# Optimization experiments

Hardware: AMD Instinct MI355X
Metric: run time of the kernel (lower is better)

## Reference

```python
import jax, jax.numpy as jnp
import numpy as np

N = 10000            # nodes
E = 320000           # edges (avg degree 32)
L = 4                # layers
S = 64               # hidden 0e multiplicity
V = 16               # hidden 1o multiplicity
EMB = 32             # node-attr embedding dim
NB = 8               # bessel basis per channel (r and v -> 2*NB edge feats)
MR = 2.5             # max_radius
DEG = 32.0           # num_neighbors
GS = S + V           # gate input scalars: 64 scalars + 16 gates
NW = S * 2 + V * 2 + V * 2   # 192 per-edge tensor-product weights
MAXT = 100           # max atom types


def _semi_unitary(K):
    # Newton-Schulz orthogonalization: K^T K -> I (semi-unitary uplift matrix)
    K = K / jnp.linalg.norm(K)
    for _ in range(10):
        K = 1.5 * K - 0.5 * K @ (K.T @ K)
    return K


def _smooth_cutoff(t):
    u = 2.0 * (t - 1.0)
    y = (1.0 - jnp.cos(jnp.pi * u)) * 0.5
    return jnp.where(u > 0, 0.0, jnp.where(u < -1.0, 1.0, y))


def _edge_geom(d):
    # d: (E,3) edge vector. Returns cutoff-weighted 1x1o SH (component norm) and bessel features.
    r = jnp.linalg.norm(d, axis=1)                       # (E,)
    sh = np.sqrt(3.0) * d / r[:, None]                   # spherical harmonics 1x1o
    attr = _smooth_cutoff(r / MR)[:, None] * sh          # (E,3)
    k = jnp.arange(1, NB + 1, dtype=jnp.float32) * jnp.pi
    feat = np.sqrt(2.0 / MR) * jnp.sin(k * (r / MR)[:, None]) / r[:, None]
    return attr, feat * np.sqrt(NB)                      # (E,3), (E,NB)


def _fctp(s, v, attr, Ws, Wv):
    # FullyConnectedTensorProduct with pure-scalar (0e) node attr == attr-weighted per-irrep linear
    os = jnp.einsum('ni,ne,oie->no', s, attr, Ws) / np.sqrt(s.shape[1] * EMB)
    ov = jnp.einsum('nim,ne,oie->nom', v, attr, Wv) / np.sqrt(v.shape[1] * EMB)
    return os, ov


def _forward(x, node_attr, edge_src, edge_dst, emb_table, PU_K, h, mix,
             si_Ws, si_Wv, sc_Ws, sc_Wv, lin1_Ws, lin1_Wv, lin2_Ws, lin2_Wv,
             fc_W1, fc_b1, fc_W2, fc_b2, fc_W3, fc_b3):
    attr = emb_table[node_attr]                          # (N,EMB)
    K = _semi_unitary(PU_K)                              # (V,2)
    yv = jnp.einsum('ui,nim->num', K, x.reshape(N, 2, 3))  # uplift vectors
    ys = jnp.zeros((N, S), x.dtype)
    ys_old, yv_old = ys, yv
    c_s, c_x = np.sin(np.pi / 8), np.cos(np.pi / 8)
    for i in range(L):
        ar, fr = _edge_geom(x[:, :3][edge_src] - x[:, :3][edge_dst])
        av, fv = _edge_geom(x[:, 3:][edge_src] - x[:, 3:][edge_dst])
        a = jnp.stack([ar, av], axis=1)                  # (E,2,3) = 2x1o edge attr
        ef = jnp.concatenate([fr, fv], axis=1)           # (E,2*NB)
        # radial MLP -> per-edge TP weights
        hd = jax.nn.silu(ef @ fc_W1[i] + fc_b1[i])
        hd = jax.nn.silu(hd @ fc_W2[i] + fc_b2[i])
        w = hd @ fc_W3[i] + fc_b3[i]                     # (E,NW)
        w1 = w[:, :S * 2].reshape(-1, S, 2)
        w2 = w[:, S * 2:S * 2 + V * 2].reshape(-1, V, 2)
        w3 = w[:, S * 2 + V * 2:].reshape(-1, V, 2)
        # conv: lin1 -> gather -> TP -> scatter -> lin2 ; plus self-connection
        fs, fvv = _fctp(ys, yv, attr, lin1_Ws[i], lin1_Wv[i])
        s_src, v_src = fs[edge_src], fvv[edge_src]
        # 0e x 1o -> 1o (uvu)
        o1 = jnp.einsum('euv,eu,evm->eum', w1, s_src, a) / np.sqrt(2.0)   # (E,S,3)
        # 1o x 1o -> 0e (uvu)
        dots = jnp.einsum('eum,evm->euv', v_src, a)
        o2 = jnp.einsum('euv,euv->eu', w2, dots) / np.sqrt(6.0)           # (E,V)
        # 1o x 1o -> 1o (cross, uvu)
        cr = jnp.cross(v_src[:, :, None, :], a[:, None, :, :])            # (E,V,2,3)
        o3 = jnp.einsum('euv,euvm->eum', w3, cr) / 2.0                    # (E,V,3)
        mid_s = jax.ops.segment_sum(o2, edge_dst, num_segments=N) / np.sqrt(DEG)
        mid_v = jax.ops.segment_sum(jnp.concatenate([o1, o3], axis=1), edge_dst,
                                    num_segments=N) / np.sqrt(DEG)        # (N,S+V,3)
        cs2, cv2 = _fctp(mid_s, mid_v, attr, lin2_Ws[i], lin2_Wv[i])      # (N,GS),(N,V,3)
        scs, scv = _fctp(ys, yv, attr, sc_Ws[i], sc_Wv[i])
        conv_s = c_s * scs + c_x * cs2
        conv_v = c_s * scv + c_x * cv2
        # gate: silu scalars, sigmoid gates * gated vectors
        gns = jax.nn.silu(conv_s[:, :S])
        gnv = jax.nn.sigmoid(conv_s[:, S:])[:, :, None] * conv_v
        # self-interaction: per-irrep linear
        sis = ys @ si_Ws[i].T / np.sqrt(S)
        siv = jnp.einsum('oi,nim->nom', si_Wv[i], yv) / np.sqrt(V)
        # leapfrog update
        h2 = h[i] ** 2
        ns = 2.0 * ys - ys_old + h2 * (mix[i] * gns + (mix[i] - 1.0) * sis)
        nv = 2.0 * yv - yv_old + h2 * (mix[i] * gnv + (mix[i] - 1.0) * siv)
        ys_old, yv_old = ys, yv
        ys, yv = ns, nv
        x = jnp.einsum('ui,num->nim', K, yv).reshape(N, 6)   # project
    return x


def setup_inputs() -> dict:
    key = jax.random.key(0)
    ks = jax.random.split(key, 24)
    def g(i, sh, fan=1.0):
        return jax.random.normal(ks[i], sh, dtype=jnp.float32) / np.sqrt(fan)
    edge_src = jax.random.randint(ks[20], (E,), 0, N, dtype=jnp.int32)
    off = jax.random.randint(ks[21], (E,), 1, N, dtype=jnp.int32)
    edge_dst = (edge_src + off) % N                      # guarantees src != dst
    return {
        'x': g(0, (N, 6)),
        'batch': jnp.zeros((N,), jnp.int32),
        'node_attr': jax.random.randint(ks[22], (N,), 0, MAXT, dtype=jnp.int32),
        'edge_src': edge_src,
        'edge_dst': edge_dst,
        'emb_table': g(1, (MAXT, EMB)),
        'PU_K': g(2, (V, 2)),
        'h': jnp.full((L,), 0.01, jnp.float32),
        'mix': jnp.full((L,), 0.5, jnp.float32),
        'si_Ws': g(3, (L, S, S)), 'si_Wv': g(4, (L, V, V)),
        'sc_Ws': g(5, (L, GS, S, EMB)), 'sc_Wv': g(6, (L, V, V, EMB)),
        'lin1_Ws': g(7, (L, S, S, EMB)), 'lin1_Wv': g(8, (L, V, V, EMB)),
        'lin2_Ws': g(9, (L, GS, V, EMB)), 'lin2_Wv': g(10, (L, V, S + V, EMB)),
        'fc_W1': g(11, (L, 2 * NB, 64), 2 * NB), 'fc_b1': jnp.zeros((L, 64), jnp.float32),
        'fc_W2': g(12, (L, 64, 64), 64), 'fc_b2': jnp.zeros((L, 64), jnp.float32),
        'fc_W3': g(13, (L, 64, NW), 64), 'fc_b3': jnp.zeros((L, NW), jnp.float32),
    }


def reference(x, batch, node_attr, edge_src, edge_dst, emb_table, PU_K, h, mix,
              si_Ws, si_Wv, sc_Ws, sc_Wv, lin1_Ws, lin1_Wv, lin2_Ws, lin2_Wv,
              fc_W1, fc_b1, fc_W2, fc_b2, fc_W3, fc_b3):
    return _forward(x, node_attr, edge_src, edge_dst, emb_table, PU_K, h, mix,
                    si_Ws, si_Wv, sc_Ws, sc_Wv, lin1_Ws, lin1_Wv, lin2_Ws, lin2_Wv,
                    fc_W1, fc_b1, fc_W2, fc_b2, fc_W3, fc_b3)
```

## Files before the change

### kernel.cpp

```cpp
#include <hip/hip_runtime.h>
#include <hip/hip_fp8.h>
#include <math.h>

#define NN 10000
#define NE 320000
#define NEP (NE + 64)
#define PI_F 3.14159265358979323846f

typedef __attribute__((ext_vector_type(8))) short short8x;
typedef __attribute__((ext_vector_type(4))) float float4x;

#if defined(__has_builtin)
#if __has_builtin(__builtin_amdgcn_cvt_pk_fp8_f32) && __has_builtin(__builtin_amdgcn_cvt_f32_fp8)
#define HW_FP8 1
#endif
#endif

__device__ __forceinline__ unsigned short f2b(float f) {
    unsigned b = __float_as_uint(f);
    return (unsigned short)((b + 0x7FFFu + ((b >> 16) & 1u)) >> 16);
}
__device__ __forceinline__ float b2f(unsigned short u) {
    return __uint_as_float(((unsigned)u) << 16);
}
__device__ __forceinline__ float silu(float x) {
    return x / (1.f + __expf(-x));
}
__device__ __forceinline__ unsigned char f2e4(float f) {
#ifdef HW_FP8
    int r = __builtin_amdgcn_cvt_pk_fp8_f32(f, f, 0, false);
    return (unsigned char)(r & 0xff);
#else
    __hip_fp8_e4m3 q(f);
    return (unsigned char)q.__x;
#endif
}
__device__ __forceinline__ unsigned short pk2(float lo, float hi) {
#ifdef HW_FP8
    int r = __builtin_amdgcn_cvt_pk_fp8_f32(lo, hi, 0, false);
    return (unsigned short)(r & 0xffff);
#else
    return (unsigned short)((unsigned)f2e4(lo) | ((unsigned)f2e4(hi) << 8));
#endif
}
__device__ __forceinline__ float e42f(unsigned char v) {
#ifdef HW_FP8
    return __builtin_amdgcn_cvt_f32_fp8((int)v, 0);
#else
    __hip_fp8_e4m3 q;
    q.__x = (__hip_fp8_storage_t)v;
    return (float)q;
#endif
}
__device__ __forceinline__ float e4sel(unsigned word, int sel) {
#ifdef HW_FP8
    switch (sel & 3) {
        case 0:  return __builtin_amdgcn_cvt_f32_fp8((int)word, 0);
        case 1:  return __builtin_amdgcn_cvt_f32_fp8((int)word, 1);
        case 2:  return __builtin_amdgcn_cvt_f32_fp8((int)word, 2);
        default: return __builtin_amdgcn_cvt_f32_fp8((int)word, 3);
    }
#else
    return e42f((unsigned char)((word >> (8*(sel & 3))) & 0xffu));
#endif
}

__global__ void k_newton_kernel(const float* __restrict__ PU, float* __restrict__ Kout)
{
    if (threadIdx.x != 0 || blockIdx.x != 0) return;
    float K[32];
    float nrm = 0.f;
    for (int i = 0; i < 32; ++i) { K[i] = PU[i]; nrm += K[i]*K[i]; }
    float inv = 1.0f / sqrtf(nrm);
    for (int i = 0; i < 32; ++i) K[i] *= inv;
    for (int it = 0; it < 10; ++it) {
        float m00 = 0.f, m01 = 0.f, m11 = 0.f;
        for (int u = 0; u < 16; ++u) {
            float a = K[2*u], b = K[2*u+1];
            m00 += a*a; m01 += a*b; m11 += b*b;
        }
        for (int u = 0; u < 16; ++u) {
            float a = K[2*u], b = K[2*u+1];
            K[2*u]   = 1.5f*a - 0.5f*(a*m00 + b*m01);
            K[2*u+1] = 1.5f*b - 0.5f*(a*m01 + b*m11);
        }
    }
    for (int i = 0; i < 32; ++i) Kout[i] = K[i];
}

__global__ __launch_bounds__(256) void init_all_kernel(
    const float* __restrict__ x, const float* __restrict__ K,
    float* __restrict__ xp, float* __restrict__ yv0, float* __restrict__ yv1,
    float* __restrict__ ys0, float* __restrict__ ys1, float* __restrict__ fsb)
{
    int tid = blockIdx.x*256 + threadIdx.x;
    if (tid < NN*8) {
        int n = tid >> 3, c = tid & 7;
        xp[tid] = (c < 6) ? x[n*6 + c] : 0.f;
        return;
    }
    int t2 = tid - NN*8;
    if (t2 < NN*48) {
        int n = t2/48, j = t2%48, u = j/3, m = j%3;
        float v = K[2*u]*x[n*6+m] + K[2*u+1]*x[n*6+3+m];
        yv0[t2] = v; yv1[t2] = v;
        return;
    }
    t2 -= NN*48;
    if (t2 < NN*64) { ys0[t2] = 0.f; ys1[t2] = 0.f; fsb[t2] = 0.f; }
}

__global__ void init_fvv_kernel(const float* __restrict__ yv, const int* __restrict__ types,
                                const float* __restrict__ lin1vT0, float* __restrict__ fvv)
{
    int tid = blockIdx.x*blockDim.x + threadIdx.x;
    if (tid >= NN*48) return;
    int n = tid/48, j = tid%48, o = j/3, m = j%3;
    int t = types[n];
    const float* W = lin1vT0 + (size_t)t*256;
    float acc = 0.f;
    #pragma unroll
    for (int i = 0; i < 16; ++i) acc += yv[n*48 + i*3 + m]*W[i*16 + o];
    fvv[tid] = acc;
}

__device__ __forceinline__ void be_body(const float* __restrict__ W, const float* __restrict__ emb,
                                        float* __restrict__ out, int id, int O, int I, float scale)
{
    int o = id % O; int r = id / O;
    int i = r % I; r /= I;
    int t = r % 100; int l = r / 100;
    const float* w  = W + (((size_t)l*O + o)*I + i)*32;
    const float* em = emb + (size_t)t*32;
    float acc = 0.f;
    #pragma unroll
    for (int e = 0; e < 32; ++e) acc += w[e]*em[e];
    out[id] = acc*scale;
}

#define PREP_TOTAL (2048000 + 1638400 + 512000 + 512000 + 102400 + 102400 + 49152 + 16384 + 16384 + 8192 + 1024)
__global__ __launch_bounds__(256) void prep_kernel(
    const float* __restrict__ lin1_Ws, const float* __restrict__ lin1_Wv,
    const float* __restrict__ sc_Ws,   const float* __restrict__ sc_Wv,
    const float* __restrict__ lin2_Ws, const float* __restrict__ lin2_Wv,
    const float* __restrict__ si_Ws,   const float* __restrict__ si_Wv,
    const float* __restrict__ fc_W1,   const float* __restrict__ fc_W2,
    const float* __restrict__ fc_W3,   const float* __restrict__ emb,
    float* __restrict__ lin1sT, float* __restrict__ lin1vT,
    float* __restrict__ scsT,   float* __restrict__ scvT,
    float* __restrict__ lin2sT, float* __restrict__ lin2vT,
    float* __restrict__ siWsT,  float* __restrict__ siWvT,
    unsigned short* __restrict__ w1bp, unsigned short* __restrict__ w2bp,
    unsigned short* __restrict__ w3bf)
{
    const float s2048 = 0.022097086912079608f;
    const float s512  = 0.044194173824159216f;
    const float s2560 = 0.019764235376052372f;
    int tid = blockIdx.x*256 + threadIdx.x;
    if (tid < 2048000) { be_body(sc_Ws,   emb, scsT,   tid, 80, 64, s2048); return; }
    tid -= 2048000;
    if (tid < 1638400) { be_body(lin1_Ws, emb, lin1sT, tid, 64, 64, s2048); return; }
    tid -= 1638400;
    if (tid < 512000)  { be_body(lin2_Ws, emb, lin2sT, tid, 80, 16, s512);  return; }
    tid -= 512000;
    if (tid < 512000)  { be_body(lin2_Wv, emb, lin2vT, tid, 16, 80, s2560); return; }
    tid -= 512000;
    if (tid < 102400)  { be_body(lin1_Wv, emb, lin1vT, tid, 16, 16, s512);  return; }
    tid -= 102400;
    if (tid < 102400)  { be_body(sc_Wv,   emb, scvT,   tid, 16, 16, s512);  return; }
    tid -= 102400;
    if (tid < 49152) {
        int o = tid % 64; int r = tid / 64; int i = r % 192; int l = r / 192;
        w3bf[tid] = f2b(fc_W3[((size_t)l*64 + o)*192 + i]);
        return;
    }
    tid -= 49152;
    if (tid < 16384) {
        int o = tid % 64; int r = tid / 64; int i = r % 64; int l = r / 64;
        siWsT[tid] = si_Ws[((size_t)l*64 + o)*64 + i]*0.125f;
        return;
    }
    tid -= 16384;
    if (tid < 16384) {
        int kk = tid % 64; int r = tid / 64; int n = r % 64; int l = r / 64;
        w2bp[tid] = f2b(fc_W2[((size_t)l*64 + kk)*64 + n]);
        return;
    }
    tid -= 16384;
    if (tid < 8192) {
        int kk = tid % 32; int r = tid / 32; int n = r % 64; int l = r / 64;
        float v = (kk < 16) ? fc_W1[((size_t)l*16 + kk)*64 + n] : 0.f;
        w1bp[tid] = f2b(v);
        return;
    }
    tid -= 8192;
    if (tid < 1024) {
        int o = tid % 16; int r = tid / 16; int i = r % 16; int l = r / 16;
        siWvT[tid] = si_Wv[((size_t)l*16 + o)*16 + i]*0.25f;
    }
}

__global__ void hist_kernel(const int* __restrict__ dst, int* __restrict__ deg)
{
    int e = blockIdx.x*256 + threadIdx.x;
    if (e < NE) atomicAdd(&deg[dst[e]], 1);
}

__global__ __launch_bounds__(256) void scan_kernel(const int* __restrict__ deg,
                                                   int* __restrict__ segoff,
                                                   int* __restrict__ cursor)
{
    __shared__ int part[256];
    int tid = threadIdx.x;
    int base = tid*40;
    int s = 0;
    for (int i = 0; i < 40; ++i) { int idx = base+i; if (idx < NN) s += deg[idx]; }
    part[tid] = s;
    __syncthreads();
    for (int o = 1; o < 256; o <<= 1) {
        int v = (tid >= o) ? part[tid-o] : 0;
        __syncthreads();
        part[tid] += v;
        __syncthreads();
    }
    int excl = part[tid] - s;
    for (int i = 0; i < 40; ++i) {
        int idx = base+i;
        if (idx < NN) { segoff[idx] = excl; cursor[idx] = excl; excl += deg[idx]; }
        else if (idx == NN) { segoff[NN] = excl; }
    }
}

__global__ void scatter_kernel(const int* __restrict__ src, const int* __restrict__ dst,
                               int* __restrict__ cursor,
                               int* __restrict__ srcs, int* __restrict__ dsts)
{
    int e = blockIdx.x*256 + threadIdx.x;
    if (e >= NE) return;
    int d = dst[e];
    int p = atomicAdd(&cursor[d], 1);
    srcs[p] = src[e]; dsts[p] = d;
}

__global__ __launch_bounds__(256, 8) void edge_fused_kernel(
    const float* __restrict__ xp,
    const int* __restrict__ srcs, const int* __restrict__ dsts,
    const unsigned short* __restrict__ w1b,
    const float* __restrict__ b1,
    const unsigned short* __restrict__ w2b,
    const float* __restrict__ b2,
    const unsigned short* __restrict__ w3b,
    const float* __restrict__ b3,
    const float* __restrict__ fs, const float* __restrict__ fvv,
    unsigned short* __restrict__ ebuf)
{
    __shared__ __align__(16) unsigned char smem[64*196];
    __shared__ float abuf[64*6];
    unsigned short* hbuf = (unsigned short*)smem;
    unsigned char*  wbuf = smem;
    int lane = threadIdx.x & 63;
    int wid  = threadIdx.x >> 6;
    int eblk = blockIdx.x * 64;
    int row16 = lane & 15, quad = lane >> 4;
    int erow = 16*wid + row16;

    if (lane < 16) {
        int p = eblk + 16*wid + lane;
        int s = srcs[p], d = dsts[p];
        const float4* xs4 = (const float4*)(xp + (size_t)s*8);
        const float4* xd4 = (const float4*)(xp + (size_t)d*8);
        float4 xsa = xs4[0], xsb = xs4[1];
        float4 xda = xd4[0], xdb = xd4[1];
        float a0[3], a1[3], ef[16];
        {
            float d0 = xsa.x-xda.x, d1 = xsa.y-xda.y, d2 = xsa.z-xda.z;
            float r = sqrtf(d0*d0 + d1*d1 + d2*d2);
            float invr = 1.0f/r;
            float u = 0.8f*r - 2.0f;
            float cut = (u > 0.f) ? 0.f : ((u < -1.f) ? 1.f : 0.5f*(1.f - __cosf(PI_F*u)));
            float sc = 1.7320508075688772f*cut*invr;
            a0[0] = sc*d0; a0[1] = sc*d1; a0[2] = sc*d2;
            float fsc = 2.5298221281347035f*invr;
            #pragma unroll
            for (int k = 0; k < 8; ++k) ef[k] = fsc*__sinf((k+1)*1.2566370614359172f*r);
        }
        {
            float d0 = xsa.w-xda.w, d1 = xsb.x-xdb.x, d2 = xsb.y-xdb.y;
            float r = sqrtf(d0*d0 + d1*d1 + d2*d2);
            float invr = 1.0f/r;
            float u = 0.8f*r - 2.0f;
            float cut = (u > 0.f) ? 0.f : ((u < -1.f) ? 1.f : 0.5f*(1.f - __cosf(PI_F*u)));
            float sc = 1.7320508075688772f*cut*invr;
            a1[0] = sc*d0; a1[1] = sc*d1; a1[2] = sc*d2;
            float fsc = 2.5298221281347035f*invr;
            #pragma unroll
            for (int k = 0; k < 8; ++k) ef[8+k] = fsc*__sinf((k+1)*1.2566370614359172f*r);
        }
        float* ab = abuf + (16*wid + lane)*6;
        ab[0] = a0[0]; ab[1] = a0[1]; ab[2] = a0[2];
        ab[3] = a1[0]; ab[4] = a1[1]; ab[5] = a1[2];
        unsigned epk[8];
        #pragma unroll
        for (int k = 0; k < 8; ++k)
            epk[k] = (unsigned)f2b(ef[2*k]) | ((unsigned)f2b(ef[2*k+1]) << 16);
        uint4* hr = (uint4*)(hbuf + (16*wid + lane)*72);
        uint4 q0; q0.x = epk[0]; q0.y = epk[1]; q0.z = epk[2]; q0.w = epk[3];
        uint4 q1; q1.x = epk[4]; q1.y = epk[5]; q1.z = epk[6]; q1.w = epk[7];
        uint4 qz; qz.x = 0; qz.y = 0; qz.z = 0; qz.w = 0;
        hr[0] = q0; hr[1] = q1; hr[2] = qz; hr[3] = qz;
    }

    {
        short8x a = *(const short8x*)(hbuf + erow*72 + quad*8);
        float4x c[4];
        #pragma unroll
        for (int nt = 0; nt < 4; ++nt) {
            short8x b = *(const short8x*)(w1b + ((size_t)(nt*16 + row16))*32 + quad*8);
            c[nt] = __builtin_amdgcn_mfma_f32_16x16x32_bf16(a, b, (float4x){0.f,0.f,0.f,0.f}, 0, 0, 0);
        }
        #pragma unroll
        for (int nt = 0; nt < 4; ++nt) {
            float bias = b1[nt*16 + row16];
            #pragma unroll
            for (int r = 0; r < 4; ++r) {
                float h = silu(c[nt][r] + bias);
                hbuf[(16*wid + quad*4 + r)*72 + nt*16 + row16] = f2b(h);
            }
        }
    }
    {
        short8x a0v = *(const short8x*)(hbuf + erow*72 + 0*32 + quad*8);
        short8x a1v = *(const short8x*)(hbuf + erow*72 + 1*32 + quad*8);
        float4x c[4];
        #pragma unroll
        for (int nt = 0; nt < 4; ++nt) {
            short8x b0 = *(const short8x*)(w2b + ((size_t)(nt*16 + row16))*64 + 0*32 + quad*8);
            float4x t = __builtin_amdgcn_mfma_f32_16x16x32_bf16(a0v, b0, (float4x){0.f,0.f,0.f,0.f}, 0, 0, 0);
            short8x b1v = *(const short8x*)(w2b + ((size_t)(nt*16 + row16))*64 + 1*32 + quad*8);
            c[nt] = __builtin_amdgcn_mfma_f32_16x16x32_bf16(a1v, b1v, t, 0, 0, 0);
        }
        #pragma unroll
        for (int nt = 0; nt < 4; ++nt) {
            float bias = b2[nt*16 + row16];
            #pragma unroll
            for (int r = 0; r < 4; ++r) {
                float h = silu(c[nt][r] + bias);
                hbuf[(16*wid + quad*4 + r)*72 + nt*16 + row16] = f2b(h);
            }
        }
    }
    {
        short8x a0v = *(const short8x*)(hbuf + erow*72 + 0*32 + quad*8);
        short8x a1v = *(const short8x*)(hbuf + erow*72 + 1*32 + quad*8);
        __syncthreads();
        float4x acc[12];
        #pragma unroll
        for (int nt = 0; nt < 12; ++nt) {
            short8x b0 = *(const short8x*)(w3b + ((size_t)(nt*16 + row16))*64 + 0*32 + quad*8);
            float4x t = __builtin_amdgcn_mfma_f32_16x16x32_bf16(a0v, b0, (float4x){0.f,0.f,0.f,0.f}, 0, 0, 0);
            short8x b1v = *(const short8x*)(w3b + ((size_t)(nt*16 + row16))*64 + 1*32 + quad*8);
            acc[nt] = __builtin_amdgcn_mfma_f32_16x16x32_bf16(a1v, b1v, t, 0, 0, 0);
        }
        #pragma unroll
        for (int nt = 0; nt < 12; ++nt) {
            #pragma unroll
            for (int r = 0; r < 4; ++r) {
                wbuf[(16*wid + quad*4 + r)*196 + nt*16 + row16] = f2e4(acc[nt][r]);
            }
        }
    }
    __syncthreads();

    int p = eblk + lane;
    const unsigned* wrow32 = (const unsigned*)(wbuf + lane*196);
    float a0[3], a1[3];
    {
        const float* ab = abuf + lane*6;
        a0[0] = ab[0]; a0[1] = ab[1]; a0[2] = ab[2];
        a1[0] = ab[3]; a1[1] = ab[4]; a1[2] = ab[5];
    }
    int s = srcs[p];
    {
        int U0 = 16*wid;
        int rbase = 24*wid;
        float fsr[16];
        {
            const float4* f4 = (const float4*)(fs + (size_t)s*64 + U0);
            #pragma unroll
            for (int g = 0; g < 4; ++g) {
                float4 t = f4[g];
                fsr[4*g+0] = t.x; fsr[4*g+1] = t.y; fsr[4*g+2] = t.z; fsr[4*g+3] = t.w;
            }
        }
        float carry = 0.f;
        #pragma unroll
        for (int uu = 0; uu < 16; ++uu) {
            int u = U0 + uu;
            float su = fsr[uu]*0.125f;
            unsigned word = wrow32[u >> 1];
            float wa = e4sel(word, (uu & 1)*2)     + b3[2*u];
            float wb = e4sel(word, (uu & 1)*2 + 1) + b3[2*u+1];
            float q0 = su*(wa*a0[0] + wb*a1[0]);
            float q1 = su*(wa*a0[1] + wb*a1[1]);
            float q2 = su*(wa*a0[2] + wb*a1[2]);
            if ((uu & 1) == 0) {
                ebuf[(size_t)(rbase + (3*uu)/2)*NEP + p] = pk2(q0, q1);
                carry = q2;
            } else {
                ebuf[(size_t)(rbase + (3*uu-1)/2)*NEP + p] = pk2(carry, q0);
                ebuf[(size_t)(rbase + (3*uu+1)/2)*NEP + p] = pk2(q1, q2);
            }
        }
    }
    {
        int U0 = 4*wid;
        float fvr[12];
        {
            const float4* f4 = (const float4*)(fvv + (size_t)s*48 + 3*U0);
            #pragma unroll
            for (int g = 0; g < 3; ++g) {
                float4 t = f4[g];
                fvr[4*g+0] = t.x; fvr[4*g+1] = t.y; fvr[4*g+2] = t.z; fvr[4*g+3] = t.w;
            }
        }
        int r2base = 96 + 2*wid;
        int r3base = 104 + 6*wid;
        float o2v[4];
        float carry = 0.f;
        #pragma unroll
        for (int uu = 0; uu < 4; ++uu) {
            int u = U0 + uu;
            float v0 = fvr[uu*3+0], v1 = fvr[uu*3+1], v2 = fvr[uu*3+2];
            unsigned w2w = wrow32[32 + (u >> 1)];
            unsigned w3w = wrow32[40 + (u >> 1)];
            float w2a = e4sel(w2w, (uu & 1)*2)     + b3[128+2*u];
            float w2b = e4sel(w2w, (uu & 1)*2 + 1) + b3[129+2*u];
            float w3a = e4sel(w3w, (uu & 1)*2)     + b3[160+2*u];
            float w3b = e4sel(w3w, (uu & 1)*2 + 1) + b3[161+2*u];
            float dd0 = v0*a0[0] + v1*a0[1] + v2*a0[2];
            float dd1 = v0*a1[0] + v1*a1[1] + v2*a1[2];
            o2v[uu] = (w2a*dd0 + w2b*dd1)*0.07216878364870323f;
            float c0x = v1*a0[2]-v2*a0[1], c0y = v2*a0[0]-v0*a0[2], c0z = v0*a0[1]-v1*a0[0];
            float c1x = v1*a1[2]-v2*a1[1], c1y = v2*a1[0]-v0*a1[2], c1z = v0*a1[1]-v1*a1[0];
            float q0 = 0.08838834764831845f*(w3a*c0x + w3b*c1x);
            float q1 = 0.08838834764831845f*(w3a*c0y + w3b*c1y);
            float q2 = 0.08838834764831845f*(w3a*c0z + w3b*c1z);
            if ((uu & 1) == 0) {
                ebuf[(size_t)(r3base + (3*uu)/2)*NEP + p] = pk2(q0, q1);
                carry = q2;
            } else {
                ebuf[(size_t)(r3base + (3*uu-1)/2)*NEP + p] = pk2(carry, q0);
                ebuf[(size_t)(r3base + (3*uu+1)/2)*NEP + p] = pk2(q1, q2);
            }
        }
        ebuf[(size_t)(r2base + 0)*NEP + p] = pk2(o2v[0], o2v[1]);
        ebuf[(size_t)(r2base + 1)*NEP + p] = pk2(o2v[2], o2v[3]);
    }
}

__global__ __launch_bounds__(256) void segsum_kernel(
    const unsigned short* __restrict__ ebuf,
    const int* __restrict__ segoff,
    float* __restrict__ mid)
{
    __shared__ int sbnd[18];
    __shared__ unsigned short stile[256*66];
    int c = threadIdx.x;
    int lane = c & 63, wid = c >> 6;
    int n0 = blockIdx.x * 16;
    if (c < 17) sbnd[c] = segoff[n0 + c];
    else if (c == 17) sbnd[17] = 0x7fffffff;
    __syncthreads();
    int P0 = sbnd[0], P1 = sbnd[16];
    int A = P0 & ~63;
    float cur = 0.f;
    int seg = 0;
    int bnext = sbnd[1];
    const unsigned short* row = stile + c*66;
    for (int base = A; base < P1; base += 64) {
        {
            const unsigned short* src = ebuf + (size_t)(32*wid)*NEP + base + lane;
            unsigned short* dst = stile + (64*wid)*66 + lane;
            #pragma unroll
            for (int rr = 0; rr < 32; ++rr) {
                unsigned v = (unsigned)src[(size_t)rr*NEP];
                dst[(2*rr  )*66] = f2b(e4sel(v, 0));
                dst[(2*rr+1)*66] = f2b(e4sel(v, 1));
            }
        }
        __syncthreads();
        int e0 = (base < P0) ? P0 : base;
        int e1 = (base + 64 < P1) ? (base + 64) : P1;
        int e = e0;
        while (e < e1) {
            int stop = (bnext < e1) ? bnext : e1;
            if (((e - base) & 1) && e < stop) { cur += b2f(row[e - base]); ++e; }
            for (; e + 2 <= stop; e += 2) {
                unsigned v = *(const unsigned*)(row + (e - base));
                cur += b2f((unsigned short)(v & 0xffffu)) + b2f((unsigned short)(v >> 16));
            }
            if (e < stop) { cur += b2f(row[e - base]); ++e; }
            if (e == bnext) {
                mid[(size_t)(n0 + seg)*256 + c] = cur;
                cur = 0.f; ++seg; bnext = sbnd[seg + 1];
            }
        }
        __syncthreads();
    }
    while (seg < 16) {
        mid[(size_t)(n0 + seg)*256 + c] = cur;
        cur = 0.f; ++seg;
    }
}

__global__ __launch_bounds__(256) void node_update_kernel(
    const float* __restrict__ ys, const float* __restrict__ yv,
    float* __restrict__ ys_old, float* __restrict__ yv_old,
    const float* __restrict__ mid,
    const int* __restrict__ types,
    const float* __restrict__ scsT, const float* __restrict__ scvT,
    const float* __restrict__ lin2sT, const float* __restrict__ lin2vT,
    const float* __restrict__ siWsT, const float* __restrict__ siWvT,
    const float* __restrict__ lin1sTn, const float* __restrict__ lin1vTn,
    const float* __restrict__ Kbuf,
    const float* __restrict__ hv, const float* __restrict__ mixv, int layer,
    float* __restrict__ fs_out, float* __restrict__ fvv_out,
    float* __restrict__ xpad, float* __restrict__ dout)
{
    int n = blockIdx.x;
    int lane = threadIdx.x;
    __shared__ float ys_l[64], yv_l[48], mids[16], midv[240];
    __shared__ float conv_s[80], conv_v[48], sis_l[64], siv_l[48], ysn[64], yvn[48];
    int t = types[n];
    {
        float v = mid[(size_t)n*256 + lane];
        if (lane < 192) midv[lane] = v;
        else if (lane < 208) mids[lane-192] = v;
        else midv[192 + (lane-208)] = v;
    }
    if (lane < 64) ys_l[lane] = ys[n*64 + lane];
    else if (lane < 112) yv_l[lane-64] = yv[n*48 + (lane-64)];
    __syncthreads();
    if (lane < 80) {
        const float* Wsc = scsT + (size_t)t*5120;
        const float* W2s = lin2sT + (size_t)t*1280;
        float a_sc = 0.f, a_2 = 0.f;
        #pragma unroll
        for (int i = 0; i < 64; ++i) a_sc += ys_l[i]*Wsc[i*80 + lane];
        #pragma unroll
        for (int i = 0; i < 16; ++i) a_2 += mids[i]*W2s[i*80 + lane];
        conv_s[lane] = 0.3826834323650898f*a_sc + 0.9238795325112867f*a_2;
    } else if (lane < 144) {
        int o = lane - 80;
        float a_si = 0.f;
        #pragma unroll
        for (int i = 0; i < 64; ++i) a_si += ys_l[i]*siWsT[i*64 + o];
        sis_l[o] = a_si;
    } else if (lane < 192) {
        int j = lane - 144, o = j/3, m = j%3;
        const float* Wsc = scvT + (size_t)t*256;
        const float* W2v = lin2vT + (size_t)t*1280;
        float a_sc = 0.f, a_2 = 0.f, a_si = 0.f;
        #pragma unroll
        for (int i = 0; i < 16; ++i) {
            float y = yv_l[i*3+m];
            a_sc += y*Wsc[i*16+o];
            a_si += y*siWvT[i*16+o];
        }
        #pragma unroll
        for (int i = 0; i < 80; ++i) a_2 += midv[i*3+m]*W2v[i*16+o];
        conv_v[j] = 0.3826834323650898f*a_sc + 0.9238795325112867f*a_2;
        siv_l[j] = a_si;
    }
    __syncthreads();
    float hh = hv[layer]; float h2c = hh*hh; float mx = mixv[layer];
    if (lane < 64) {
        float cs = conv_s[lane];
        float gns = cs/(1.f + __expf(-cs));
        float ns = 2.f*ys_l[lane] - ys_old[n*64+lane] + h2c*(mx*gns + (mx-1.f)*sis_l[lane]);
        ys_old[n*64+lane] = ns;
        ysn[lane] = ns;
    } else if (lane < 112) {
        int j = lane-64, o = j/3;
        float g = 1.f/(1.f + __expf(-conv_s[64+o]));
        float gnv = g*conv_v[j];
        float nv = 2.f*yv_l[j] - yv_old[n*48+j] + h2c*(mx*gnv + (mx-1.f)*siv_l[j]);
        yv_old[n*48+j] = nv;
        yvn[j] = nv;
    }
    __syncthreads();
    if (lane < 6) {
        int i = lane/3, m = lane%3;
        float acc = 0.f;
        #pragma unroll
        for (int u = 0; u < 16; ++u) acc += Kbuf[2*u+i]*yvn[u*3+m];
        xpad[n*8 + lane] = acc;
        if (dout) dout[n*6 + lane] = acc;
    }
    if (lane < 64) {
        const float* W = lin1sTn + (size_t)t*4096;
        float acc = 0.f;
        #pragma unroll
        for (int i = 0; i < 64; ++i) acc += ysn[i]*W[i*64 + lane];
        fs_out[n*64 + lane] = acc;
    } else if (lane < 112) {
        int j = lane - 64, o = j/3, m = j%3;
        const float* W = lin1vTn + (size_t)t*256;
        float acc = 0.f;
        #pragma unroll
        for (int i = 0; i < 16; ++i) acc += yvn[i*3+m]*W[i*16 + o];
        fvv_out[n*48 + j] = acc;
    }
}

extern "C" void kernel_launch(void* const* d_in, const int* in_sizes, int n_in,
                              void* d_out, int out_size, void* d_ws, size_t ws_size,
                              hipStream_t stream)
{
    const float* x_in   = (const float*)d_in[0];
    const int*   types  = (const int*)  d_in[2];
    const int*   esrc   = (const int*)  d_in[3];
    const int*   edst   = (const int*)  d_in[4];
    const float* emb    = (const float*)d_in[5];
    const float* PU     = (const float*)d_in[6];
    const float* hv     = (const float*)d_in[7];
    const float* mixv   = (const float*)d_in[8];
    const float* si_Ws  = (const float*)d_in[9];
    const float* si_Wv  = (const float*)d_in[10];
    const float* sc_Ws  = (const float*)d_in[11];
    const float* sc_Wv  = (const float*)d_in[12];
    const float* lin1_Ws= (const float*)d_in[13];
    const float* lin1_Wv= (const float*)d_in[14];
    const float* lin2_Ws= (const float*)d_in[15];
    const float* lin2_Wv= (const float*)d_in[16];
    const float* fc_W1  = (const float*)d_in[17];
    const float* fc_b1  = (const float*)d_in[18];
    const float* fc_W2  = (const float*)d_in[19];
    const float* fc_b2  = (const float*)d_in[20];
    const float* fc_W3  = (const float*)d_in[21];
    const float* fc_b3  = (const float*)d_in[22];

    float* ws = (float*)d_ws;
    size_t off = 0;
    auto alloc = [&](size_t nf) { float* p = ws + off; off += nf; return p; };
    float* Kbuf   = alloc(64);
    float* x_pad  = alloc(80000);
    float* ys0    = alloc(640000);
    float* ys1    = alloc(640000);
    float* yv0    = alloc(480000);
    float* yv1    = alloc(480000);
    float* fsb    = alloc(640000);
    float* fvvb   = alloc(480000);
    float* midb   = alloc((size_t)NN*256);
    float* lin1sT = alloc((size_t)4*100*4096);
    float* lin1vT = alloc((size_t)4*100*256);
    float* scsT   = alloc((size_t)4*100*5120);
    float* scvT   = alloc((size_t)4*100*256);
    float* lin2sT = alloc((size_t)4*100*1280);
    float* lin2vT = alloc((size_t)4*100*1280);
    float* siWsT  = alloc((size_t)4*4096);
    float* siWvT  = alloc((size_t)4*256);
    int* iws = (int*)(ws + off);
    size_t ioff = 0;
    auto ialloc = [&](size_t ni) { int* p = iws + ioff; ioff += ni; return p; };
    int* deg    = ialloc(NN);
    int* segoff = ialloc(NN + 8);
    int* cursor = ialloc(NN);
    int* srcs   = ialloc(NE);
    int* dsts   = ialloc(NE);
    unsigned short* w1bp = (unsigned short*)(iws + ioff);
    unsigned short* w2bp = w1bp + (size_t)4*64*32;
    unsigned short* w3bf = w2bp + (size_t)4*64*64;
    unsigned short* ebuf = w3bf + (size_t)4*192*64;

    k_newton_kernel<<<1, 1, 0, stream>>>(PU, Kbuf);
    prep_kernel<<<(PREP_TOTAL + 255)/256, 256, 0, stream>>>(
        lin1_Ws, lin1_Wv, sc_Ws, sc_Wv, lin2_Ws, lin2_Wv, si_Ws, si_Wv,
        fc_W1, fc_W2, fc_W3, emb,
        lin1sT, lin1vT, scsT, scvT, lin2sT, lin2vT, siWsT, siWvT,
        w1bp, w2bp, w3bf);
    {
        int tot = NN*8 + NN*48 + NN*64;
        init_all_kernel<<<(tot + 255)/256, 256, 0, stream>>>(
            x_in, Kbuf, x_pad, yv0, yv1, ys0, ys1, fsb);
    }
    init_fvv_kernel<<<(NN*48 + 255)/256, 256, 0, stream>>>(yv0, types, lin1vT, fvvb);

    (void)hipMemsetAsync(deg, 0, NN*sizeof(int), stream);
    hist_kernel<<<(NE+255)/256, 256, 0, stream>>>(edst, deg);
    scan_kernel<<<1, 256, 0, stream>>>(deg, segoff, cursor);
    scatter_kernel<<<(NE+255)/256, 256, 0, stream>>>(esrc, edst, cursor, srcs, dsts);

    float* ys_cur = ys0; float* ys_old = ys1;
    float* yv_cur = yv0; float* yv_old = yv1;
    for (int l = 0; l < 4; ++l) {
        edge_fused_kernel<<<NE/64, 256, 0, stream>>>(
            x_pad, srcs, dsts,
            w1bp + (size_t)l*64*32,  fc_b1 + (size_t)l*64,
            w2bp + (size_t)l*64*64,  fc_b2 + (size_t)l*64,
            w3bf + (size_t)l*192*64, fc_b3 + (size_t)l*192,
            fsb, fvvb, ebuf);
        segsum_kernel<<<NN/16, 256, 0, stream>>>(ebuf, segoff, midb);
        int ln = (l + 1) & 3;
        node_update_kernel<<<NN, 256, 0, stream>>>(
            ys_cur, yv_cur, ys_old, yv_old,
            midb, types,
            scsT   + (size_t)l*100*5120, scvT   + (size_t)l*100*256,
            lin2sT + (size_t)l*100*1280, lin2vT + (size_t)l*100*1280,
            siWsT  + (size_t)l*4096,     siWvT  + (size_t)l*256,
            lin1sT + (size_t)ln*100*4096, lin1vT + (size_t)ln*100*256,
            Kbuf, hv, mixv, l, fsb, fvvb,
            x_pad, (l == 3) ? (float*)d_out : nullptr);
        float* tmp;
        tmp = ys_cur; ys_cur = ys_old; ys_old = tmp;
        tmp = yv_cur; yv_cur = yv_old; yv_old = tmp;
    }
}
```

Measured before the change: 1.044 ms.

## Sort nodes by atom type for weight locality; spread edge geometry across all threads

Adds a single-block counting sort of nodes by atom type and has node_update process blocks in that order, so consecutive blocks share the same per-type weight matrices and hit in cache. The edge kernel's geometry and Bessel feature computation is split across all 256 threads (4 per edge) instead of 16 lanes per wave, with an explicit barrier added. The extra sort kernel is small but serial, and the atomic ordering within a type bucket is nondeterministic, which only changes processing order.

```diff
diff --git a/kernel.cpp b/kernel.cpp
--- a/kernel.cpp
+++ b/kernel.cpp
@@ -242,6 +242,26 @@
     srcs[p] = src[e]; dsts[p] = d;
 }
 
+__global__ __launch_bounds__(256) void nsort_kernel(const int* __restrict__ types,
+                                                    int* __restrict__ nperm)
+{
+    __shared__ int hist[100], base[100];
+    int t = threadIdx.x;
+    if (t < 100) hist[t] = 0;
+    __syncthreads();
+    for (int n = t; n < NN; n += 256) atomicAdd(&hist[types[n]], 1);
+    __syncthreads();
+    if (t == 0) {
+        int acc = 0;
+        for (int i = 0; i < 100; ++i) { base[i] = acc; acc += hist[i]; }
+    }
+    __syncthreads();
+    for (int n = t; n < NN; n += 256) {
+        int p = atomicAdd(&base[types[n]], 1);
+        nperm[p] = n;
+    }
+}
+
 __global__ __launch_bounds__(256, 8) void edge_fused_kernel(
     const float* __restrict__ xp,
     const int* __restrict__ srcs, const int* __restrict__ dsts,
@@ -264,51 +284,45 @@
     int row16 = lane & 15, quad = lane >> 4;
     int erow = 16*wid + row16;
 
-    if (lane < 16) {
-        int p = eblk + 16*wid + lane;
+    {
+        int c = threadIdx.x;
+        int e = c >> 2, j = c & 3;
+        int p = eblk + e;
         int s = srcs[p], d = dsts[p];
         const float4* xs4 = (const float4*)(xp + (size_t)s*8);
         const float4* xd4 = (const float4*)(xp + (size_t)d*8);
-        float4 xsa = xs4[0], xsb = xs4[1];
-        float4 xda = xd4[0], xdb = xd4[1];
-        float a0[3], a1[3], ef[16];
-        {
-            float d0 = xsa.x-xda.x, d1 = xsa.y-xda.y, d2 = xsa.z-xda.z;
-            float r = sqrtf(d0*d0 + d1*d1 + d2*d2);
-            float invr = 1.0f/r;
+        float d0, d1, d2;
+        if (j < 2) {
+            float4 xsa = xs4[0], xda = xd4[0];
+            d0 = xsa.x-xda.x; d1 = xsa.y-xda.y; d2 = xsa.z-xda.z;
+        } else {
+            float4 xsa = xs4[0], xsb = xs4[1];
+            float4 xda = xd4[0], xdb = xd4[1];
+            d0 = xsa.w-xda.w; d1 = xsb.x-xdb.x; d2 = xsb.y-xdb.y;
+        }
+        float r = sqrtf(d0*d0 + d1*d1 + d2*d2);
+        float invr = 1.0f/r;
+        if ((j & 1) == 0) {
             float u = 0.8f*r - 2.0f;
             float cut = (u > 0.f) ? 0.f : ((u < -1.f) ? 1.f : 0.5f*(1.f - __cosf(PI_F*u)));
             float sc = 1.7320508075688772f*cut*invr;
-            a0[0] = sc*d0; a0[1] = sc*d1; a0[2] = sc*d2;
-            float fsc = 2.5298221281347035f*invr;
-            #pragma unroll
-            for (int k = 0; k < 8; ++k) ef[k] = fsc*__sinf((k+1)*1.2566370614359172f*r);
-        }
-        {
-            float d0 = xsa.w-xda.w, d1 = xsb.x-xdb.x, d2 = xsb.y-xdb.y;
-            float r = sqrtf(d0*d0 + d1*d1 + d2*d2);
-            float invr = 1.0f/r;
-            float u = 0.8f*r - 2.0f;
-            float cut = (u > 0.f) ? 0.f : ((u < -1.f) ? 1.f : 0.5f*(1.f - __cosf(PI_F*u)));
-            float sc = 1.7320508075688772f*cut*invr;
-            a1[0] = sc*d0; a1[1] = sc*d1; a1[2] = sc*d2;
-            float fsc = 2.5298221281347035f*invr;
-            #pragma unroll
-            for (int k = 0; k < 8; ++k) ef[8+k] = fsc*__sinf((k+1)*1.2566370614359172f*r);
-        }
-        float* ab = abuf + (16*wid + lane)*6;
-        ab[0] = a0[0]; ab[1] = a0[1]; ab[2] = a0[2];
-        ab[3] = a1[0]; ab[4] = a1[1]; ab[5] = a1[2];
-        unsigned epk[8];
-        #pragma unroll
-        for (int k = 0; k < 8; ++k)
-            epk[k] = (unsigned)f2b(ef[2*k]) | ((unsigned)f2b(ef[2*k+1]) << 16);
-        uint4* hr = (uint4*)(hbuf + (16*wid + lane)*72);
-        uint4 q0; q0.x = epk[0]; q0.y = epk[1]; q0.z = epk[2]; q0.w = epk[3];
-        uint4 q1; q1.x = epk[4]; q1.y = epk[5]; q1.z = epk[6]; q1.w = epk[7];
-        uint4 qz; qz.x = 0; qz.y = 0; qz.z = 0; qz.w = 0;
-        hr[0] = q0; hr[1] = q1; hr[2] = qz; hr[3] = qz;
-    }
+            float* ab = abuf + e*6 + (j >> 1)*3;
+            ab[0] = sc*d0; ab[1] = sc*d1; ab[2] = sc*d2;
+        }
+        float fsc = 2.5298221281347035f*invr;
+        int kb = (j & 1)*4;
+        float v0 = fsc*__sinf((kb+1)*1.2566370614359172f*r);
+        float v1 = fsc*__sinf((kb+2)*1.2566370614359172f*r);
+        float v2 = fsc*__sinf((kb+3)*1.2566370614359172f*r);
+        float v3 = fsc*__sinf((kb+4)*1.2566370614359172f*r);
+        uint2 q;
+        q.x = (unsigned)f2b(v0) | ((unsigned)f2b(v1) << 16);
+        q.y = (unsigned)f2b(v2) | ((unsigned)f2b(v3) << 16);
+        *(uint2*)(hbuf + e*72 + j*4) = q;
+        uint2 z; z.x = 0; z.y = 0;
+        *(uint2*)(hbuf + e*72 + 16 + j*4) = z;
+    }
+    __syncthreads();
 
     {
         short8x a = *(const short8x*)(hbuf + erow*72 + quad*8);
@@ -517,7 +531,7 @@
     const float* __restrict__ ys, const float* __restrict__ yv,
     float* __restrict__ ys_old, float* __restrict__ yv_old,
     const float* __restrict__ mid,
-    const int* __restrict__ types,
+    const int* __restrict__ types, const int* __restrict__ nperm,
     const float* __restrict__ scsT, const float* __restrict__ scvT,
     const float* __restrict__ lin2sT, const float* __restrict__ lin2vT,
     const float* __restrict__ siWsT, const float* __restrict__ siWvT,
@@ -527,7 +541,7 @@
     float* __restrict__ fs_out, float* __restrict__ fvv_out,
     float* __restrict__ xpad, float* __restrict__ dout)
 {
-    int n = blockIdx.x;
+    int n = nperm[blockIdx.x];
     int lane = threadIdx.x;
     __shared__ float ys_l[64], yv_l[48], mids[16], midv[240];
     __shared__ float conv_s[80], conv_v[48], sis_l[64], siv_l[48], ysn[64], yvn[48];
@@ -668,6 +682,7 @@
     int* cursor = ialloc(NN);
     int* srcs   = ialloc(NE);
     int* dsts   = ialloc(NE);
+    int* nperm  = ialloc(NN + 8);
     unsigned short* w1bp = (unsigned short*)(iws + ioff);
     unsigned short* w2bp = w1bp + (size_t)4*64*32;
     unsigned short* w3bf = w2bp + (size_t)4*64*64;
@@ -690,6 +705,7 @@
     hist_kernel<<<(NE+255)/256, 256, 0, stream>>>(edst, deg);
     scan_kernel<<<1, 256, 0, stream>>>(deg, segoff, cursor);
     scatter_kernel<<<(NE+255)/256, 256, 0, stream>>>(esrc, edst, cursor, srcs, dsts);
+    nsort_kernel<<<1, 256, 0, stream>>>(types, nperm);
 
     float* ys_cur = ys0; float* ys_old = ys1;
     float* yv_cur = yv0; float* yv_old = yv1;
@@ -704,7 +720,7 @@
         int ln = (l + 1) & 3;
         node_update_kernel<<<NN, 256, 0, stream>>>(
             ys_cur, yv_cur, ys_old, yv_old,
-            midb, types,
+            midb, types, nperm,
             scsT   + (size_t)l*100*5120, scvT   + (size_t)l*100*256,
             lin2sT + (size_t)l*100*1280, lin2vT + (size_t)l*100*1280,
             siWsT  + (size_t)l*4096,     siWvT  + (size_t)l*256,
```

After: 1.064 ms. No clear change (+2.0%).
